# Performance work log

Measured on AMD Instinct MI355X. Metric: run time of the kernel, lower is better.

Reference implementation:

```python
import jax, jax.numpy as jnp
import numpy as np

B, S, DIN, DH = 8, 4096, 1024, 1024


def setup_inputs() -> dict:
    key = jax.random.key(0)
    k1, k2, k3, k4 = jax.random.split(key, 4)
    x = jax.random.normal(k1, (B, S, DIN), jnp.float32)
    # previous hidden state must be strictly positive (log-domain scan)
    h = jax.random.uniform(k2, (B, 1, DH), jnp.float32, minval=0.05, maxval=0.95)
    W = jax.random.normal(k3, (2 * DH, DIN), jnp.float32) * (1.0 / np.sqrt(DIN))
    b = jax.random.normal(k4, (2 * DH,), jnp.float32) * 0.01
    return {"x": x, "h": h, "W": W, "b": b}


def _log_g(x):
    # log of g(x) = x + 0.5 if x >= 0 else sigmoid(x)
    return jnp.where(x >= 0, jnp.log(jnp.where(x >= 0, x, 0.0) + 0.5), -jax.nn.softplus(-x))


def reference(x, h, W, b):
    # gate/hidden projection: (B,S,2H)
    gh = jnp.einsum('bsi,oi->bso', x, W) + b
    gate, hidden = jnp.split(gh, 2, axis=2)  # each (B,S,H)

    # minGRU recurrence h_t = (1-z_t) h_{t-1} + z_t g(hidden_t), z_t = sigmoid(gate_t)
    # evaluated with the Heinsen log-space parallel scan
    log_z = -jax.nn.softplus(-gate)        # log sigmoid(gate)
    log_coeffs = -jax.nn.softplus(gate)    # log (1 - sigmoid(gate))
    log_h0 = jnp.log(h)                    # (B,1,H)
    log_values = jnp.concatenate([log_h0, log_z + _log_g(hidden)], axis=1)  # (B,S+1,H)

    a_star = jnp.cumsum(jnp.pad(log_coeffs, ((0, 0), (1, 0), (0, 0))), axis=1)  # (B,S+1,H)
    log_h = a_star + jax.lax.cumlogsumexp(log_values - a_star, axis=1)
    return jnp.exp(log_h)[:, 1:]  # (B,S,H)
```

## Files before the change

### kernel.cpp

```cpp
#include <hip/hip_runtime.h>

typedef __attribute__((ext_vector_type(4))) float f32x4;
typedef __attribute__((ext_vector_type(8))) short short8;

#define M_TOT 32768
#define N_TOT 2048
#define K_TOT 1024
#define NCHUNK 64
#define CLEN 64

__device__ __forceinline__ unsigned short f2bf(float f) {
    union { float f; unsigned int u; } a; a.f = f;
    unsigned int r = a.u + 0x7fffu + ((a.u >> 16) & 1u);
    return (unsigned short)(r >> 16);
}
__device__ __forceinline__ float bf2f(unsigned short u) {
    union { unsigned int u; float f; } a; a.u = ((unsigned int)u) << 16;
    return a.f;
}

__global__ __launch_bounds__(256) void conv_bf16(const float* __restrict__ in,
                                                 unsigned short* __restrict__ out, int n4) {
    int stride = gridDim.x * 256;
    for (int i = blockIdx.x * 256 + threadIdx.x; i < n4; i += stride) {
        float4 v = reinterpret_cast<const float4*>(in)[i];
        ushort4 o;
        o.x = f2bf(v.x); o.y = f2bf(v.y); o.z = f2bf(v.z); o.w = f2bf(v.w);
        reinterpret_cast<ushort4*>(out)[i] = o;
    }
}

__global__ __launch_bounds__(256) void gemm_act(
    const unsigned short* __restrict__ xb, const unsigned short* __restrict__ wb,
    const float* __restrict__ bias,
    unsigned short* __restrict__ zA, unsigned short* __restrict__ G)
{
    __shared__ unsigned short lA[128 * 32];
    __shared__ unsigned short lB[128 * 32];
    const int bid = blockIdx.x;
    const int nt = bid & 15;
    const int mt = bid >> 4;
    const int m0 = mt * 128, n0 = nt * 128;
    const int t = threadIdx.x;
    const int w = t >> 6, l = t & 63;

    f32x4 acc[4][4];
#pragma unroll
    for (int i = 0; i < 4; ++i)
#pragma unroll
        for (int j = 0; j < 4; ++j) acc[i][j] = (f32x4){0.f, 0.f, 0.f, 0.f};

    const unsigned short* ga = xb + (m0 + (t >> 2)) * 1024 + (t & 3) * 8;
    const unsigned short* gb = wb + (n0 + (t >> 2)) * 1024 + (t & 3) * 8;
    unsigned short* la0 = &lA[t * 8];
    unsigned short* la1 = &lA[2048 + t * 8];
    unsigned short* lb0 = &lB[t * 8];
    unsigned short* lb1 = &lB[2048 + t * 8];

    const int wr = (w >> 1) * 64, wc = (w & 1) * 64;
    const unsigned short* pa = &lA[(wr + (l & 15)) * 32 + (l >> 4) * 8];
    const unsigned short* pb = &lB[(wc + (l & 15)) * 32 + (l >> 4) * 8];

    for (int kt = 0; kt < 32; ++kt) {
        __syncthreads();
        const unsigned short* gak = ga + kt * 32;
        const unsigned short* gbk = gb + kt * 32;
        __builtin_amdgcn_global_load_lds((const __attribute__((address_space(1))) unsigned int*)gak,
                                         (__attribute__((address_space(3))) unsigned int*)la0, 16, 0, 0);
        __builtin_amdgcn_global_load_lds((const __attribute__((address_space(1))) unsigned int*)(gak + 64 * 1024),
                                         (__attribute__((address_space(3))) unsigned int*)la1, 16, 0, 0);
        __builtin_amdgcn_global_load_lds((const __attribute__((address_space(1))) unsigned int*)gbk,
                                         (__attribute__((address_space(3))) unsigned int*)lb0, 16, 0, 0);
        __builtin_amdgcn_global_load_lds((const __attribute__((address_space(1))) unsigned int*)(gbk + 64 * 1024),
                                         (__attribute__((address_space(3))) unsigned int*)lb1, 16, 0, 0);
        asm volatile("s_waitcnt vmcnt(0)" ::: "memory");
        __syncthreads();

        short8 af[4], bfr[4];
#pragma unroll
        for (int i = 0; i < 4; ++i) af[i]  = *reinterpret_cast<const short8*>(pa + i * 16 * 32);
#pragma unroll
        for (int i = 0; i < 4; ++i) bfr[i] = *reinterpret_cast<const short8*>(pb + i * 16 * 32);
#pragma unroll
        for (int mi = 0; mi < 4; ++mi)
#pragma unroll
            for (int ni = 0; ni < 4; ++ni)
                acc[mi][ni] = __builtin_amdgcn_mfma_f32_16x16x32_bf16(af[mi], bfr[ni], acc[mi][ni], 0, 0, 0);
    }

    const int col = l & 15;
    const int rbase = (l >> 4) * 4;
#pragma unroll
    for (int ni = 0; ni < 4; ++ni) {
        int gc = n0 + wc + ni * 16 + col;
        float bv = bias[gc];
        bool isGate = gc < 1024;
        unsigned short* dst = isGate ? zA : G;
        int cc = isGate ? gc : (gc - 1024);
#pragma unroll
        for (int mi = 0; mi < 4; ++mi) {
            int gr = m0 + wr + mi * 16 + rbase;
#pragma unroll
            for (int r = 0; r < 4; ++r) {
                float v = acc[mi][ni][r] + bv;
                float o;
                if (isGate) o = 1.f / (1.f + __expf(-v));
                else        o = (v >= 0.f) ? (v + 0.5f) : 1.f / (1.f + __expf(-v));
                dst[(gr + r) * 1024 + cc] = f2bf(o);
            }
        }
    }
}

__global__ __launch_bounds__(256) void scan_carry(
    const unsigned short* __restrict__ zA, const unsigned short* __restrict__ G,
    float* __restrict__ CC, float* __restrict__ CV)
{
    int g = blockIdx.x * 256 + threadIdx.x;
    int hp = g & 511;
    int ck = (g >> 9) & 63;
    int b  = g >> 15;
    int mbase = b * 4096 + ck * CLEN;
    const unsigned int* pa = (const unsigned int*)zA + (size_t)mbase * 512 + hp;
    const unsigned int* pg = (const unsigned int*)G  + (size_t)mbase * 512 + hp;
    float C0 = 1.f, V0 = 0.f, C1 = 1.f, V1 = 0.f;
#pragma unroll 8
    for (int i = 0; i < CLEN; ++i) {
        unsigned int ua = pa[i * 512];
        unsigned int ug = pg[i * 512];
        float a0 = bf2f(ua & 0xffff), a1 = bf2f(ua >> 16);
        float g0 = bf2f(ug & 0xffff), g1 = bf2f(ug >> 16);
        float c0 = 1.f - a0, c1 = 1.f - a1;
        C0 *= c0; V0 = c0 * V0 + a0 * g0;
        C1 *= c1; V1 = c1 * V1 + a1 * g1;
    }
    int idx = (b * 64 + ck) * 1024 + hp * 2;
    *reinterpret_cast<float2*>(CC + idx) = make_float2(C0, C1);
    *reinterpret_cast<float2*>(CV + idx) = make_float2(V0, V1);
}

__global__ __launch_bounds__(256) void scan_prefix(
    const float* __restrict__ CC, const float* __restrict__ CV,
    const float* __restrict__ h0, float* __restrict__ Hinit)
{
    int g = blockIdx.x * 256 + threadIdx.x;
    int h = g & 1023, b = g >> 10;
    float hc = h0[b * 1024 + h];
#pragma unroll 4
    for (int ck = 0; ck < NCHUNK; ++ck) {
        int idx = (b * 64 + ck) * 1024 + h;
        Hinit[idx] = hc;
        hc = CC[idx] * hc + CV[idx];
    }
}

__global__ __launch_bounds__(256) void scan_apply(
    const unsigned short* __restrict__ zA, const unsigned short* __restrict__ G,
    const float* __restrict__ Hinit, float* __restrict__ out)
{
    int g = blockIdx.x * 256 + threadIdx.x;
    int hp = g & 511;
    int ck = (g >> 9) & 63;
    int b  = g >> 15;
    int mbase = b * 4096 + ck * CLEN;
    const unsigned int* pa = (const unsigned int*)zA + (size_t)mbase * 512 + hp;
    const unsigned int* pg = (const unsigned int*)G  + (size_t)mbase * 512 + hp;
    float2 hh = *reinterpret_cast<const float2*>(Hinit + (b * 64 + ck) * 1024 + hp * 2);
    float h0v = hh.x, h1v = hh.y;
    float2* po = reinterpret_cast<float2*>(out) + (size_t)mbase * 512 + hp;
#pragma unroll 8
    for (int i = 0; i < CLEN; ++i) {
        unsigned int ua = pa[i * 512];
        unsigned int ug = pg[i * 512];
        float a0 = bf2f(ua & 0xffff), a1 = bf2f(ua >> 16);
        float g0 = bf2f(ug & 0xffff), g1 = bf2f(ug >> 16);
        h0v = (1.f - a0) * h0v + a0 * g0;
        h1v = (1.f - a1) * h1v + a1 * g1;
        po[i * 512] = make_float2(h0v, h1v);
    }
}

extern "C" void kernel_launch(void* const* d_in, const int* in_sizes, int n_in,
                              void* d_out, int out_size, void* d_ws, size_t ws_size,
                              hipStream_t stream)
{
    const float* x    = (const float*)d_in[0];
    const float* h0   = (const float*)d_in[1];
    const float* W    = (const float*)d_in[2];
    const float* bias = (const float*)d_in[3];
    float* out = (float*)d_out;

    unsigned short* xb = (unsigned short*)d_out;

    unsigned short* wb = (unsigned short*)d_ws;
    unsigned short* zA = wb + (size_t)2097152;
    unsigned short* G  = zA + (size_t)33554432;
    float* CC    = (float*)(G + (size_t)33554432);
    float* CV    = CC + 524288;
    float* Hinit = CV + 524288;

    conv_bf16<<<2048, 256, 0, stream>>>(x, xb, 33554432 / 4);
    conv_bf16<<<512, 256, 0, stream>>>(W, wb, 2097152 / 4);
    gemm_act<<<4096, 256, 0, stream>>>(xb, wb, bias, zA, G);
    scan_carry<<<1024, 256, 0, stream>>>(zA, G, CC, CV);
    scan_prefix<<<32, 256, 0, stream>>>(CC, CV, h0, Hinit);
    scan_apply<<<1024, 256, 0, stream>>>(zA, G, Hinit, out);
}
```

Before: 501.1 us.

## Fuse chunk-carry scan into GEMM epilogue with interleaved gate/hidden weight tiles

The gate and hidden weight rows are permuted so each 256-column GEMM tile holds matching gate and hidden channels. That lets the epilogue compute packed (1-z, z*g) coefficients and the per-chunk carry directly from LDS, which removes the separate scan_carry pass and one full re-read of the activations. The GEMM moves to 256x256 tiles with 512 threads, a triple-buffered async LDS pipeline, XOR swizzling and a block-index swizzle, all aimed at higher MFMA utilization. The extra bf16 rounding of the coefficients is mirrored in the carry so the two stay consistent, at the cost of heavy LDS use (96KB) and more complex code.

```diff
diff --git a/kernel.cpp b/kernel.cpp
--- a/kernel.cpp
+++ b/kernel.cpp
@@ -3,9 +3,6 @@
 typedef __attribute__((ext_vector_type(4))) float f32x4;
 typedef __attribute__((ext_vector_type(8))) short short8;
 
-#define M_TOT 32768
-#define N_TOT 2048
-#define K_TOT 1024
 #define NCHUNK 64
 #define CLEN 64
 
@@ -30,113 +27,169 @@
     }
 }
 
-__global__ __launch_bounds__(256) void gemm_act(
-    const unsigned short* __restrict__ xb, const unsigned short* __restrict__ wb,
+__global__ __launch_bounds__(256) void conv_w_perm(const float* __restrict__ in,
+                                                   unsigned short* __restrict__ out) {
+    int i = blockIdx.x * 256 + threadIdx.x;
+    int r = i >> 8, c4 = i & 255;
+    float4 v = reinterpret_cast<const float4*>(in)[i];
+    int rp;
+    if (r < 1024) { rp = (r >> 7) * 256 + (r & 127); }
+    else { int ch = r - 1024; rp = (ch >> 7) * 256 + 128 + (ch & 127); }
+    ushort4 o;
+    o.x = f2bf(v.x); o.y = f2bf(v.y); o.z = f2bf(v.z); o.w = f2bf(v.w);
+    reinterpret_cast<ushort4*>(out)[rp * 256 + c4] = o;
+}
+
+__global__ __launch_bounds__(512, 2) void gemm_fused(
+    const unsigned short* __restrict__ xb, const unsigned short* __restrict__ wbP,
     const float* __restrict__ bias,
-    unsigned short* __restrict__ zA, unsigned short* __restrict__ G)
-{
-    __shared__ unsigned short lA[128 * 32];
-    __shared__ unsigned short lB[128 * 32];
+    unsigned int* __restrict__ CVg, float* __restrict__ CCc, float* __restrict__ CVc)
+{
+    __shared__ char lds[98304];
     const int bid = blockIdx.x;
-    const int nt = bid & 15;
-    const int mt = bid >> 4;
-    const int m0 = mt * 128, n0 = nt * 128;
+    const int swz = (bid & 7) * 128 + (bid >> 3);
+    const int nt = swz & 7, mt = swz >> 3;
+    const int m0 = mt * 256, chBase = nt * 128, n0p = nt * 256;
     const int t = threadIdx.x;
     const int w = t >> 6, l = t & 63;
-
-    f32x4 acc[4][4];
-#pragma unroll
-    for (int i = 0; i < 4; ++i)
-#pragma unroll
-        for (int j = 0; j < 4; ++j) acc[i][j] = (f32x4){0.f, 0.f, 0.f, 0.f};
-
-    const unsigned short* ga = xb + (m0 + (t >> 2)) * 1024 + (t & 3) * 8;
-    const unsigned short* gb = wb + (n0 + (t >> 2)) * 1024 + (t & 3) * 8;
-    unsigned short* la0 = &lA[t * 8];
-    unsigned short* la1 = &lA[2048 + t * 8];
-    unsigned short* lb0 = &lB[t * 8];
-    unsigned short* lb1 = &lB[2048 + t * 8];
-
-    const int wr = (w >> 1) * 64, wc = (w & 1) * 64;
-    const unsigned short* pa = &lA[(wr + (l & 15)) * 32 + (l >> 4) * 8];
-    const unsigned short* pb = &lB[(wc + (l & 15)) * 32 + (l >> 4) * 8];
-
-    for (int kt = 0; kt < 32; ++kt) {
-        __syncthreads();
-        const unsigned short* gak = ga + kt * 32;
-        const unsigned short* gbk = gb + kt * 32;
-        __builtin_amdgcn_global_load_lds((const __attribute__((address_space(1))) unsigned int*)gak,
-                                         (__attribute__((address_space(3))) unsigned int*)la0, 16, 0, 0);
-        __builtin_amdgcn_global_load_lds((const __attribute__((address_space(1))) unsigned int*)(gak + 64 * 1024),
-                                         (__attribute__((address_space(3))) unsigned int*)la1, 16, 0, 0);
-        __builtin_amdgcn_global_load_lds((const __attribute__((address_space(1))) unsigned int*)gbk,
-                                         (__attribute__((address_space(3))) unsigned int*)lb0, 16, 0, 0);
-        __builtin_amdgcn_global_load_lds((const __attribute__((address_space(1))) unsigned int*)(gbk + 64 * 1024),
-                                         (__attribute__((address_space(3))) unsigned int*)lb1, 16, 0, 0);
-        asm volatile("s_waitcnt vmcnt(0)" ::: "memory");
-        __syncthreads();
-
-        short8 af[4], bfr[4];
-#pragma unroll
-        for (int i = 0; i < 4; ++i) af[i]  = *reinterpret_cast<const short8*>(pa + i * 16 * 32);
-#pragma unroll
-        for (int i = 0; i < 4; ++i) bfr[i] = *reinterpret_cast<const short8*>(pb + i * 16 * 32);
-#pragma unroll
-        for (int mi = 0; mi < 4; ++mi)
+    const int wr = (w >> 2) * 128, wc = (w & 3) * 64;
+
+    const int srow = t >> 2;
+    const int scol = (t & 3) ^ ((t >> 3) & 3);
+    const unsigned short* gA = xb + (size_t)(m0 + srow) * 1024 + scol * 8;
+    const unsigned short* gB = wbP + (size_t)(n0p + srow) * 1024 + scol * 8;
+    const int sdst = t * 16;
+
+    int offA[8], offB[4];
+#pragma unroll
+    for (int mi = 0; mi < 8; ++mi) {
+        int ar = wr + mi * 16 + (l & 15);
+        int sl = (l >> 4) ^ ((ar >> 1) & 3);
+        offA[mi] = ar * 64 + sl * 16;
+    }
+#pragma unroll
+    for (int ni = 0; ni < 4; ++ni) {
+        int br = wc + ni * 16 + (l & 15);
+        int sl = (l >> 4) ^ ((br >> 1) & 3);
+        offB[ni] = br * 64 + sl * 16;
+    }
+
+    f32x4 acc[8][4];
+#pragma unroll
+    for (int mi = 0; mi < 8; ++mi)
+#pragma unroll
+        for (int ni = 0; ni < 4; ++ni) acc[mi][ni] = (f32x4){0.f, 0.f, 0.f, 0.f};
+
+    auto stage = [&](int tile, int buf) {
+        const unsigned short* a = gA + tile * 32;
+        const unsigned short* b = gB + tile * 32;
+        char* dA = lds + buf * 16384 + sdst;
+        char* dB = lds + 49152 + buf * 16384 + sdst;
+        __builtin_amdgcn_global_load_lds((const __attribute__((address_space(1))) unsigned int*)a,
+                                         (__attribute__((address_space(3))) unsigned int*)dA, 16, 0, 0);
+        __builtin_amdgcn_global_load_lds((const __attribute__((address_space(1))) unsigned int*)(a + 128 * 1024),
+                                         (__attribute__((address_space(3))) unsigned int*)(dA + 8192), 16, 0, 0);
+        __builtin_amdgcn_global_load_lds((const __attribute__((address_space(1))) unsigned int*)b,
+                                         (__attribute__((address_space(3))) unsigned int*)dB, 16, 0, 0);
+        __builtin_amdgcn_global_load_lds((const __attribute__((address_space(1))) unsigned int*)(b + 128 * 1024),
+                                         (__attribute__((address_space(3))) unsigned int*)(dB + 8192), 16, 0, 0);
+    };
+
+    stage(0, 0); stage(1, 1); stage(2, 2);
+    asm volatile("s_waitcnt vmcnt(8)" ::: "memory");
+    __builtin_amdgcn_sched_barrier(0);
+    __builtin_amdgcn_s_barrier();
+
+    int buf = 0;
+    for (int k = 0; k < 32; ++k) {
+        const char* bA = lds + buf * 16384;
+        const char* bB = lds + 49152 + buf * 16384;
+        short8 af[8], bfr[4];
+#pragma unroll
+        for (int mi = 0; mi < 8; ++mi) af[mi] = *reinterpret_cast<const short8*>(bA + offA[mi]);
+#pragma unroll
+        for (int ni = 0; ni < 4; ++ni) bfr[ni] = *reinterpret_cast<const short8*>(bB + offB[ni]);
+        asm volatile("s_waitcnt lgkmcnt(0)" ::: "memory");
+        __builtin_amdgcn_sched_barrier(0);
+        __builtin_amdgcn_s_barrier();
+        if (k < 29) stage(k + 3, buf);
+        __builtin_amdgcn_s_setprio(1);
+#pragma unroll
+        for (int mi = 0; mi < 8; ++mi)
 #pragma unroll
             for (int ni = 0; ni < 4; ++ni)
                 acc[mi][ni] = __builtin_amdgcn_mfma_f32_16x16x32_bf16(af[mi], bfr[ni], acc[mi][ni], 0, 0, 0);
-    }
-
-    const int col = l & 15;
-    const int rbase = (l >> 4) * 4;
+        __builtin_amdgcn_s_setprio(0);
+        if (k <= 28)      asm volatile("s_waitcnt vmcnt(8)" ::: "memory");
+        else if (k == 29) asm volatile("s_waitcnt vmcnt(4)" ::: "memory");
+        else if (k == 30) asm volatile("s_waitcnt vmcnt(0)" ::: "memory");
+        __builtin_amdgcn_sched_barrier(0);
+        __builtin_amdgcn_s_barrier();
+        buf = (buf == 2) ? 0 : buf + 1;
+    }
+
+    const bool isGate = (wc < 128);
+    float bv[4];
 #pragma unroll
     for (int ni = 0; ni < 4; ++ni) {
-        int gc = n0 + wc + ni * 16 + col;
-        float bv = bias[gc];
-        bool isGate = gc < 1024;
-        unsigned short* dst = isGate ? zA : G;
-        int cc = isGate ? gc : (gc - 1024);
-#pragma unroll
-        for (int mi = 0; mi < 4; ++mi) {
-            int gr = m0 + wr + mi * 16 + rbase;
-#pragma unroll
-            for (int r = 0; r < 4; ++r) {
-                float v = acc[mi][ni][r] + bv;
-                float o;
-                if (isGate) o = 1.f / (1.f + __expf(-v));
-                else        o = (v >= 0.f) ? (v + 0.5f) : 1.f / (1.f + __expf(-v));
-                dst[(gr + r) * 1024 + cc] = f2bf(o);
+        int j = wc + ni * 16 + (l & 15);
+        bv[ni] = bias[isGate ? (chBase + j) : (1024 + chBase + (j - 128))];
+    }
+    const int slotw = (wr != 0);
+    for (int p = 0; p < 2; ++p) {
+        if (p) __syncthreads();
+#pragma unroll
+        for (int mi = 4 * p; mi < 4 * p + 4; ++mi) {
+#pragma unroll
+            for (int ni = 0; ni < 4; ++ni) {
+#pragma unroll
+                for (int r = 0; r < 4; ++r) {
+                    float v = acc[mi][ni][r] + bv[ni];
+                    float o = isGate ? (1.f / (1.f + __expf(-v)))
+                                     : ((v >= 0.f) ? (v + 0.5f) : (1.f / (1.f + __expf(-v))));
+                    int rr = (mi - 4 * p) * 16 + ((l >> 4) << 2) + r;
+                    int j = wc + ni * 16 + (l & 15);
+                    unsigned short* zb = (unsigned short*)lds + slotw * 16384;
+                    if (isGate) zb[rr * 128 + j] = f2bf(o);
+                    else        zb[8192 + rr * 128 + (j - 128)] = f2bf(o);
+                }
             }
         }
-    }
-}
-
-__global__ __launch_bounds__(256) void scan_carry(
-    const unsigned short* __restrict__ zA, const unsigned short* __restrict__ G,
-    float* __restrict__ CC, float* __restrict__ CV)
-{
-    int g = blockIdx.x * 256 + threadIdx.x;
-    int hp = g & 511;
-    int ck = (g >> 9) & 63;
-    int b  = g >> 15;
-    int mbase = b * 4096 + ck * CLEN;
-    const unsigned int* pa = (const unsigned int*)zA + (size_t)mbase * 512 + hp;
-    const unsigned int* pg = (const unsigned int*)G  + (size_t)mbase * 512 + hp;
-    float C0 = 1.f, V0 = 0.f, C1 = 1.f, V1 = 0.f;
+        __syncthreads();
+        {
+            int slot = t >> 8;
+            int tt = t & 255;
+            int cglob = (slot ? 2 : 0) + p;
+            int mrow0 = m0 + cglob * 64;
+            const unsigned short* zb = (const unsigned short*)lds + slot * 16384;
+            const unsigned short* gb = zb + 8192;
+            int ch = tt & 127, half = tt >> 7;
+#pragma unroll 4
+            for (int i = 0; i < 32; ++i) {
+                int rr = half * 32 + i;
+                float z = bf2f(zb[rr * 128 + ch]);
+                float gg = bf2f(gb[rr * 128 + ch]);
+                unsigned short cb = f2bf(1.f - z);
+                unsigned short vb = f2bf(z * gg);
+                CVg[(size_t)(mrow0 + rr) * 1024 + chBase + ch] =
+                    (unsigned int)cb | ((unsigned int)vb << 16);
+            }
+            if (tt < 128) {
+                float C = 1.f, V = 0.f;
 #pragma unroll 8
-    for (int i = 0; i < CLEN; ++i) {
-        unsigned int ua = pa[i * 512];
-        unsigned int ug = pg[i * 512];
-        float a0 = bf2f(ua & 0xffff), a1 = bf2f(ua >> 16);
-        float g0 = bf2f(ug & 0xffff), g1 = bf2f(ug >> 16);
-        float c0 = 1.f - a0, c1 = 1.f - a1;
-        C0 *= c0; V0 = c0 * V0 + a0 * g0;
-        C1 *= c1; V1 = c1 * V1 + a1 * g1;
-    }
-    int idx = (b * 64 + ck) * 1024 + hp * 2;
-    *reinterpret_cast<float2*>(CC + idx) = make_float2(C0, C1);
-    *reinterpret_cast<float2*>(CV + idx) = make_float2(V0, V1);
+                for (int i = 0; i < 64; ++i) {
+                    float z = bf2f(zb[i * 128 + tt]);
+                    float gg = bf2f(gb[i * 128 + tt]);
+                    float c = bf2f(f2bf(1.f - z));
+                    float vv = bf2f(f2bf(z * gg));
+                    C *= c; V = c * V + vv;
+                }
+                int b = mrow0 >> 12, ck = (mrow0 >> 6) & 63;
+                CCc[(size_t)(b * 64 + ck) * 1024 + chBase + tt] = C;
+                CVc[(size_t)(b * 64 + ck) * 1024 + chBase + tt] = V;
+            }
+        }
+    }
 }
 
 __global__ __launch_bounds__(256) void scan_prefix(
@@ -146,7 +199,7 @@
     int g = blockIdx.x * 256 + threadIdx.x;
     int h = g & 1023, b = g >> 10;
     float hc = h0[b * 1024 + h];
-#pragma unroll 4
+#pragma unroll 8
     for (int ck = 0; ck < NCHUNK; ++ck) {
         int idx = (b * 64 + ck) * 1024 + h;
         Hinit[idx] = hc;
@@ -155,28 +208,20 @@
 }
 
 __global__ __launch_bounds__(256) void scan_apply(
-    const unsigned short* __restrict__ zA, const unsigned short* __restrict__ G,
-    const float* __restrict__ Hinit, float* __restrict__ out)
+    const unsigned int* __restrict__ CVg, const float* __restrict__ Hinit,
+    float* __restrict__ out)
 {
     int g = blockIdx.x * 256 + threadIdx.x;
-    int hp = g & 511;
-    int ck = (g >> 9) & 63;
-    int b  = g >> 15;
+    int ch = g & 1023, ck = (g >> 10) & 63, b = g >> 16;
     int mbase = b * 4096 + ck * CLEN;
-    const unsigned int* pa = (const unsigned int*)zA + (size_t)mbase * 512 + hp;
-    const unsigned int* pg = (const unsigned int*)G  + (size_t)mbase * 512 + hp;
-    float2 hh = *reinterpret_cast<const float2*>(Hinit + (b * 64 + ck) * 1024 + hp * 2);
-    float h0v = hh.x, h1v = hh.y;
-    float2* po = reinterpret_cast<float2*>(out) + (size_t)mbase * 512 + hp;
+    const unsigned int* pc = CVg + (size_t)mbase * 1024 + ch;
+    float h = Hinit[g];
+    float* po = out + (size_t)mbase * 1024 + ch;
 #pragma unroll 8
     for (int i = 0; i < CLEN; ++i) {
-        unsigned int ua = pa[i * 512];
-        unsigned int ug = pg[i * 512];
-        float a0 = bf2f(ua & 0xffff), a1 = bf2f(ua >> 16);
-        float g0 = bf2f(ug & 0xffff), g1 = bf2f(ug >> 16);
-        h0v = (1.f - a0) * h0v + a0 * g0;
-        h1v = (1.f - a1) * h1v + a1 * g1;
-        po[i * 512] = make_float2(h0v, h1v);
+        unsigned int u = pc[i * 1024];
+        h = bf2f((unsigned short)(u & 0xffff)) * h + bf2f((unsigned short)(u >> 16));
+        po[i * 1024] = h;
     }
 }
 
@@ -191,18 +236,15 @@
     float* out = (float*)d_out;
 
     unsigned short* xb = (unsigned short*)d_out;
-
-    unsigned short* wb = (unsigned short*)d_ws;
-    unsigned short* zA = wb + (size_t)2097152;
-    unsigned short* G  = zA + (size_t)33554432;
-    float* CC    = (float*)(G + (size_t)33554432);
-    float* CV    = CC + 524288;
-    float* Hinit = CV + 524288;
-
-    conv_bf16<<<2048, 256, 0, stream>>>(x, xb, 33554432 / 4);
-    conv_bf16<<<512, 256, 0, stream>>>(W, wb, 2097152 / 4);
-    gemm_act<<<4096, 256, 0, stream>>>(xb, wb, bias, zA, G);
-    scan_carry<<<1024, 256, 0, stream>>>(zA, G, CC, CV);
-    scan_prefix<<<32, 256, 0, stream>>>(CC, CV, h0, Hinit);
-    scan_apply<<<1024, 256, 0, stream>>>(zA, G, Hinit, out);
-}
+    unsigned short* wbP = (unsigned short*)d_ws;
+    unsigned int* CVg = (unsigned int*)((char*)d_ws + 4194304);
+    float* CCc   = (float*)((char*)d_ws + 138412032);
+    float* CVc   = (float*)((char*)d_ws + 140509184);
+    float* Hinit = (float*)((char*)d_ws + 142606336);
+
+    conv_bf16<<<2048, 256, 0, stream>>>(x, xb, 8388608);
+    conv_w_perm<<<2048, 256, 0, stream>>>(W, wbP);
+    gemm_fused<<<1024, 512, 0, stream>>>(xb, wbP, bias, CVg, CCc, CVc);
+    scan_prefix<<<32, 256, 0, stream>>>(CCc, CVc, h0, Hinit);
+    scan_apply<<<2048, 256, 0, stream>>>(CVg, Hinit, out);
+}
```

After: 632.1 us. +26.1%, slower.
